# Kernel optimization log

Measured on AMD Instinct MI355X. Metric: run time of the kernel, lower is better.

Reference implementation:

```python
import jax, jax.numpy as jnp
import numpy as np

N = 65536   # num nodes
F = 512     # input feature dim
H = 256     # hid_dim
E = 1048576 # num edges (avg degree 16)
R = 512     # num_reps


def setup_inputs() -> dict:
    key = jax.random.key(0)
    ks = jax.random.split(key, 8)
    nodes = jax.random.normal(ks[0], (N, F), dtype=jnp.float32)
    c_nodes = jax.random.normal(ks[1], (N, F), dtype=jnp.float32)  # corrupted features
    senders = jax.random.randint(ks[2], (E,), 0, N, dtype=jnp.int32)
    receivers = jax.random.randint(ks[3], (E,), 0, N, dtype=jnp.int32)
    s = 1.0 / np.sqrt(F)
    W = jax.random.uniform(ks[4], (F, H), jnp.float32, -s, s)  # Dense kernel
    b = jnp.zeros((H,), jnp.float32)                            # Dense bias
    W_bilinear = jax.random.normal(ks[5], (H, H), jnp.float32) / np.sqrt(H)
    centers = jax.random.normal(ks[6], (R, H), jnp.float32)     # EucCluster param
    return dict(nodes=nodes, c_nodes=c_nodes, senders=senders, receivers=receivers,
                W=W, b=b, W_bilinear=W_bilinear, centers=centers)


def _gcn(x, senders, receivers, W, b):
    # jraph.GraphConvolution(Dense, add_self_edges=False, symmetric_normalization=True)
    x = x @ W + b  # [N,H]
    ones = jnp.ones((senders.shape[0],), x.dtype)
    deg_s = jax.ops.segment_sum(ones, senders, num_segments=N)
    x = x * jax.lax.rsqrt(jnp.maximum(deg_s, 1.0))[:, None]
    x = jax.ops.segment_sum(x[senders], receivers, num_segments=N)  # scatter-sum aggregation
    deg_r = jax.ops.segment_sum(ones, receivers, num_segments=N)
    x = x * jax.lax.rsqrt(jnp.maximum(deg_r, 1.0))[:, None]
    return jax.nn.selu(x)  # activation 'SeLU'


def reference(nodes, c_nodes, senders, receivers, W, b, W_bilinear, centers):
    # DGI with shared single-layer GCN (train=False path; single layer => no dropout)
    nodes1 = _gcn(nodes, senders, receivers, W, b)    # [N,H]
    nodes2 = _gcn(c_nodes, senders, receivers, W, b)  # [N,H]
    summary = jax.nn.sigmoid(jnp.mean(nodes1, axis=0))  # dgi_readout, [H]
    all_nodes = jnp.concatenate([nodes1, nodes2], axis=0)  # [2N,H]
    logits = (all_nodes @ W_bilinear) @ summary  # bilinear, [2N]
    # row L2-normalize embeddings
    emb = nodes1 / jnp.linalg.norm(nodes1, axis=1, keepdims=True)
    # Euclidean clustering: pairwise dists via GEMM trick
    d2 = (jnp.sum(emb * emb, axis=1)[:, None]
          + jnp.sum(centers * centers, axis=1)[None, :]
          - 2.0 * emb @ centers.T)  # [N,R]
    dists = jnp.sqrt(jnp.maximum(d2, 1e-12))
    cluster_dists = jnp.min(dists, axis=1)   # per-node dist to nearest center
    rep_ids = jnp.argmin(dists, axis=0)      # representative node per center
    cluster_loss = jnp.sum(cluster_dists)
    return emb, centers, rep_ids, cluster_loss, logits
```

## Files before the change

kernel.cpp:

```cpp
#include <hip/hip_runtime.h>
#include <math.h>

#define N_NODES 65536
#define F_DIM 512
#define H_DIM 256
#define E_EDGES 1048576
#define R_REPS 512

typedef _Float16 f16x8 __attribute__((ext_vector_type(8)));
typedef float f32x4_t __attribute__((ext_vector_type(4)));

__device__ __forceinline__ float selu_f(float x) {
    const float SC = 1.0507009873554804934f;
    const float AL = 1.6732632423543772848f;
    return x > 0.f ? SC * x : SC * AL * expm1f(x);
}

__device__ __forceinline__ void split8(const float* __restrict__ g, f16x8* hi, f16x8* lo) {
    float4 v0 = *(const float4*)g;
    float4 v1 = *(const float4*)(g + 4);
    f16x8 h, l;
    h[0] = (_Float16)v0.x; h[1] = (_Float16)v0.y; h[2] = (_Float16)v0.z; h[3] = (_Float16)v0.w;
    h[4] = (_Float16)v1.x; h[5] = (_Float16)v1.y; h[6] = (_Float16)v1.z; h[7] = (_Float16)v1.w;
    l[0] = (_Float16)(v0.x - (float)h[0]); l[1] = (_Float16)(v0.y - (float)h[1]);
    l[2] = (_Float16)(v0.z - (float)h[2]); l[3] = (_Float16)(v0.w - (float)h[3]);
    l[4] = (_Float16)(v1.x - (float)h[4]); l[5] = (_Float16)(v1.y - (float)h[5]);
    l[6] = (_Float16)(v1.z - (float)h[6]); l[7] = (_Float16)(v1.w - (float)h[7]);
    *hi = h; *lo = l;
}

__device__ __forceinline__ int wave_sort64(int v, int lane) {
    #pragma unroll
    for (int k = 2; k <= 64; k <<= 1) {
        #pragma unroll
        for (int j = k >> 1; j > 0; j >>= 1) {
            int p = __shfl_xor(v, j);
            bool takeMin = (((lane & j) == 0) == ((lane & k) == 0));
            int mn = min(v, p), mx = max(v, p);
            v = takeMin ? mn : mx;
        }
    }
    return v;
}

__global__ void k_init(int* cnt_s, int* cnt_r, float* colsum,
                       unsigned* node_min, unsigned long long* center_min,
                       double* loss_acc) {
    int i = blockIdx.x * 256 + threadIdx.x;
    if (i < N_NODES) { cnt_s[i] = 0; cnt_r[i] = 0; node_min[i] = 0x7F800000u; }
    if (i < H_DIM) colsum[i] = 0.f;
    if (i < R_REPS) center_min[i] = ~0ull;
    if (i == 0) *loss_acc = 0.0;
}

__global__ void k_degree(const int* __restrict__ senders, const int* __restrict__ receivers,
                         int* __restrict__ cnt_s, int* __restrict__ cnt_r) {
    int e = blockIdx.x * 256 + threadIdx.x;
    if (e < E_EDGES) {
        atomicAdd(&cnt_s[senders[e]], 1);
        atomicAdd(&cnt_r[receivers[e]], 1);
    }
}

__global__ void k_invsqrt(const int* __restrict__ cnt_s, const int* __restrict__ cnt_r,
                          float* __restrict__ inv_s, float* __restrict__ inv_r) {
    int i = blockIdx.x * 256 + threadIdx.x;
    if (i < N_NODES) {
        inv_s[i] = 1.0f / sqrtf(fmaxf((float)cnt_s[i], 1.f));
        inv_r[i] = 1.0f / sqrtf(fmaxf((float)cnt_r[i], 1.f));
    }
}

__global__ __launch_bounds__(1024) void k_scan(const int* __restrict__ cnt,
                                               int* __restrict__ row_ptr,
                                               int* __restrict__ cursor) {
    __shared__ int part[1024];
    int t = threadIdx.x;
    int base = t * 64;
    int s = 0;
    #pragma unroll 8
    for (int i = 0; i < 64; ++i) s += cnt[base + i];
    part[t] = s;
    __syncthreads();
    for (int off = 1; off < 1024; off <<= 1) {
        int other = (t >= off) ? part[t - off] : 0;
        __syncthreads();
        part[t] += other;
        __syncthreads();
    }
    int run = part[t] - s;
    for (int i = 0; i < 64; ++i) {
        row_ptr[base + i] = run;
        cursor[base + i] = run;
        run += cnt[base + i];
    }
    if (t == 1023) row_ptr[N_NODES] = run;
}

__global__ void k_fill(const int* __restrict__ senders, const int* __restrict__ receivers,
                       int* __restrict__ cursor, int* __restrict__ csr_send) {
    int e = blockIdx.x * 256 + threadIdx.x;
    if (e < E_EDGES) {
        int pos = atomicAdd(&cursor[receivers[e]], 1);
        csr_send[pos] = senders[e];
    }
}

__global__ void k_splitWT(const float* __restrict__ W, _Float16* __restrict__ hiT,
                          _Float16* __restrict__ loT) {
    int idx = blockIdx.x * 256 + threadIdx.x;
    int n = idx & (H_DIM - 1);
    int k = idx >> 8;
    float x = W[(size_t)k * H_DIM + n];
    _Float16 h = (_Float16)x;
    hiT[(size_t)n * F_DIM + k] = h;
    loT[(size_t)n * F_DIM + k] = (_Float16)(x - (float)h);
}

#define LDP 44

#define MFMA3(accv, AH, AL, BH, BL) \
    accv = __builtin_amdgcn_mfma_f32_16x16x32_f16(AH, BH, accv, 0, 0, 0); \
    accv = __builtin_amdgcn_mfma_f32_16x16x32_f16(AH, BL, accv, 0, 0, 0); \
    accv = __builtin_amdgcn_mfma_f32_16x16x32_f16(AL, BH, accv, 0, 0, 0);

#define MFMA_CORE \
    f16x8 ah[4], al[4]; \
    _Pragma("unroll") \
    for (int mi = 0; mi < 4; ++mi) { \
        ah[mi] = *(f16x8*)&Ah[wm * 64 + mi * 16 + lrow][kg * 8]; \
        al[mi] = *(f16x8*)&Al[wm * 64 + mi * 16 + lrow][kg * 8]; \
    } \
    _Pragma("unroll") \
    for (int ni = 0; ni < 4; ++ni) { \
        f16x8 bh = *(f16x8*)&Bh[wn * 64 + ni * 16 + lrow][kg * 8]; \
        f16x8 bl = *(f16x8*)&Bl[wn * 64 + ni * 16 + lrow][kg * 8]; \
        _Pragma("unroll") \
        for (int mi = 0; mi < 4; ++mi) { MFMA3(acc[mi][ni], ah[mi], al[mi], bh, bl) } \
    }

#define STAGE_A_F32(gA) { \
    f16x8 h0, l0, h1, l1; \
    split8((gA) + k0, &h0, &l0); \
    split8((gA) + k0 + 8, &h1, &l1); \
    *(f16x8*)&Ah[sr][skh] = h0; *(f16x8*)&Ah[sr][skh + 8] = h1; \
    *(f16x8*)&Al[sr][skh] = l0; *(f16x8*)&Al[sr][skh + 8] = l1; }

#define STAGE_B_F32(gB) { \
    f16x8 h0, l0, h1, l1; \
    split8((gB) + k0, &h0, &l0); \
    split8((gB) + k0 + 8, &h1, &l1); \
    *(f16x8*)&Bh[sr][skh] = h0; *(f16x8*)&Bh[sr][skh + 8] = h1; \
    *(f16x8*)&Bl[sr][skh] = l0; *(f16x8*)&Bl[sr][skh + 8] = l1; }

__global__ __launch_bounds__(256) void k_gemm_mfma(
    const float* __restrict__ A,
    const _Float16* __restrict__ BThi, const _Float16* __restrict__ BTlo,
    const float* __restrict__ bias, const float* __restrict__ inv_s,
    float* __restrict__ X, int K) {
    __shared__ _Float16 Ah[128][LDP], Al[128][LDP], Bh[128][LDP], Bl[128][LDP];
    const int t = threadIdx.x;
    const int lane = t & 63;
    const int wm = (t >> 6) >> 1, wn = (t >> 6) & 1;
    const int lrow = lane & 15, kg = lane >> 4;
    const int m0 = blockIdx.x * 128, n0 = blockIdx.y * 128;
    const int sr = t >> 1, skh = (t & 1) << 4;
    const float* gA = A + (size_t)(m0 + sr) * K + skh;
    const _Float16* gBh = BThi + (size_t)(n0 + sr) * K + skh;
    const _Float16* gBl = BTlo + (size_t)(n0 + sr) * K + skh;
    f32x4_t acc[4][4] = {};
    for (int k0 = 0; k0 < K; k0 += 32) {
        __syncthreads();
        STAGE_A_F32(gA)
        *(float4*)&Bh[sr][skh]     = *(const float4*)(gBh + k0);
        *(float4*)&Bh[sr][skh + 8] = *(const float4*)(gBh + k0 + 8);
        *(float4*)&Bl[sr][skh]     = *(const float4*)(gBl + k0);
        *(float4*)&Bl[sr][skh + 8] = *(const float4*)(gBl + k0 + 8);
        __syncthreads();
        MFMA_CORE
    }
    #pragma unroll
    for (int ni = 0; ni < 4; ++ni) {
        int col = n0 + wn * 64 + ni * 16 + lrow;
        float bc = bias[col];
        #pragma unroll
        for (int mi = 0; mi < 4; ++mi) {
            #pragma unroll
            for (int j = 0; j < 4; ++j) {
                int row = m0 + wm * 64 + mi * 16 + kg * 4 + j;
                X[(size_t)row * H_DIM + col] = (acc[mi][ni][j] + bc) * inv_s[row];
            }
        }
    }
}

__global__ __launch_bounds__(256) void k_cluster_mfma(
    const float* __restrict__ emb, const float* __restrict__ centers,
    const float* __restrict__ e2, const float* __restrict__ c2,
    unsigned* __restrict__ node_min, unsigned long long* __restrict__ center_min) {
    __shared__ _Float16 Ah[128][LDP], Al[128][LDP], Bh[128][LDP], Bl[128][LDP];
    __shared__ unsigned s_nmin[128];
    __shared__ unsigned long long s_cmin[128];
    const int t = threadIdx.x;
    const int lane = t & 63;
    const int wm = (t >> 6) >> 1, wn = (t >> 6) & 1;
    const int lrow = lane & 15, kg = lane >> 4;
    const int m0 = blockIdx.x * 128, n0 = blockIdx.y * 128;
    const int sr = t >> 1, skh = (t & 1) << 4;
    const int K = H_DIM;
    const float* gA = emb + (size_t)(m0 + sr) * K + skh;
    const float* gB = centers + (size_t)(n0 + sr) * K + skh;
    if (t < 128) { s_nmin[t] = 0x7F800000u; s_cmin[t] = ~0ull; }
    f32x4_t acc[4][4] = {};
    for (int k0 = 0; k0 < K; k0 += 32) {
        __syncthreads();
        STAGE_A_F32(gA)
        STAGE_B_F32(gB)
        __syncthreads();
        MFMA_CORE
    }
    float cv[4];
    #pragma unroll
    for (int ni = 0; ni < 4; ++ni) cv[ni] = c2[n0 + wn * 64 + ni * 16 + lrow];
    unsigned long long cb[4] = {~0ull, ~0ull, ~0ull, ~0ull};
    #pragma unroll
    for (int mi = 0; mi < 4; ++mi) {
        #pragma unroll
        for (int j = 0; j < 4; ++j) {
            int lr = wm * 64 + mi * 16 + kg * 4 + j;
            int row = m0 + lr;
            float ev = e2[row];
            float rmin = 3.402823466e+38f;
            #pragma unroll
            for (int ni = 0; ni < 4; ++ni) {
                float d2 = ev + cv[ni] - 2.f * acc[mi][ni][j];
                float d = sqrtf(fmaxf(d2, 1e-12f));
                rmin = fminf(rmin, d);
                unsigned long long pk = ((unsigned long long)__float_as_uint(d) << 32) | (unsigned)row;
                if (pk < cb[ni]) cb[ni] = pk;
            }
            atomicMin(&s_nmin[lr], __float_as_uint(rmin));
        }
    }
    #pragma unroll
    for (int ni = 0; ni < 4; ++ni)
        atomicMin(&s_cmin[wn * 64 + ni * 16 + lrow], cb[ni]);
    __syncthreads();
    if (t < 128) {
        atomicMin(&node_min[m0 + t], s_nmin[t]);
        atomicMin(&center_min[n0 + t], s_cmin[t]);
    }
}

__global__ __launch_bounds__(256) void k_agg1(
    const float* __restrict__ X, const int* __restrict__ csr_send,
    const int* __restrict__ row_ptr, const float* __restrict__ inv_r,
    float* __restrict__ out_emb) {
    int node = blockIdx.x * 4 + (threadIdx.x >> 6);
    int lane = threadIdx.x & 63;
    int beg = row_ptr[node], end = row_ptr[node + 1];
    float4 acc = {0.f, 0.f, 0.f, 0.f};
    for (int b = beg; b < end; b += 64) {
        int n = min(64, end - b);
        int myS = (lane < n) ? csr_send[b + lane] : 0x7FFFFFFF;
        myS = wave_sort64(myS, lane);
        for (int i = 0; i < n; ++i) {
            int s = __shfl(myS, i);
            float4 x = *(const float4*)&X[(size_t)s * H_DIM + (lane << 2)];
            acc.x += x.x; acc.y += x.y; acc.z += x.z; acc.w += x.w;
        }
    }
    float ir = inv_r[node];
    float4 o;
    o.x = selu_f(acc.x * ir);
    o.y = selu_f(acc.y * ir);
    o.z = selu_f(acc.z * ir);
    o.w = selu_f(acc.w * ir);
    *(float4*)&out_emb[(size_t)node * H_DIM + (lane << 2)] = o;
}

__global__ __launch_bounds__(256) void k_agg2(
    const float* __restrict__ X, const int* __restrict__ csr_send,
    const int* __restrict__ row_ptr, const float* __restrict__ inv_r,
    const float* __restrict__ v, float* __restrict__ out) {
    int node = blockIdx.x * 4 + (threadIdx.x >> 6);
    int lane = threadIdx.x & 63;
    int beg = row_ptr[node], end = row_ptr[node + 1];
    float4 acc = {0.f, 0.f, 0.f, 0.f};
    for (int b = beg; b < end; b += 64) {
        int n = min(64, end - b);
        int myS = (lane < n) ? csr_send[b + lane] : 0x7FFFFFFF;
        myS = wave_sort64(myS, lane);
        for (int i = 0; i < n; ++i) {
            int s = __shfl(myS, i);
            float4 x = *(const float4*)&X[(size_t)s * H_DIM + (lane << 2)];
            acc.x += x.x; acc.y += x.y; acc.z += x.z; acc.w += x.w;
        }
    }
    float ir = inv_r[node];
    float4 vv = *(const float4*)&v[lane << 2];
    float d = selu_f(acc.x * ir) * vv.x + selu_f(acc.y * ir) * vv.y
            + selu_f(acc.z * ir) * vv.z + selu_f(acc.w * ir) * vv.w;
    #pragma unroll
    for (int off = 32; off; off >>= 1) d += __shfl_down(d, off);
    if (lane == 0) out[node] = d;
}

__global__ __launch_bounds__(256) void k_colsum(const float* __restrict__ nodes1,
                                                float* __restrict__ colsum) {
    int t = threadIdx.x;
    size_t r0 = (size_t)blockIdx.x * 64;
    float s = 0.f;
    for (int r = 0; r < 64; ++r) s += nodes1[(r0 + r) * H_DIM + t];
    atomicAdd(&colsum[t], s);
}

__global__ void k_summary_v(const float* __restrict__ colsum, const float* __restrict__ Wb,
                            float* __restrict__ v) {
    __shared__ float s_sum[H_DIM];
    int t = threadIdx.x;
    float m = colsum[t] * (1.f / (float)N_NODES);
    s_sum[t] = 1.f / (1.f + expf(-m));
    __syncthreads();
    float acc = 0.f;
    for (int j = 0; j < H_DIM; ++j) acc += Wb[t * H_DIM + j] * s_sum[j];
    v[t] = acc;
}

__global__ __launch_bounds__(256) void k_normrow(
    float* __restrict__ emb, const float* __restrict__ v,
    float* __restrict__ logits, float* __restrict__ e2) {
    int row = blockIdx.x * 4 + (threadIdx.x >> 6);
    int lane = threadIdx.x & 63;
    float4 a = *(float4*)&emb[(size_t)row * H_DIM + (lane << 2)];
    float4 vv = *(const float4*)&v[lane << 2];
    float d = a.x * vv.x + a.y * vv.y + a.z * vv.z + a.w * vv.w;
    float ss = a.x * a.x + a.y * a.y + a.z * a.z + a.w * a.w;
    #pragma unroll
    for (int off = 32; off; off >>= 1) {
        d += __shfl_xor(d, off);
        ss += __shfl_xor(ss, off);
    }
    if (lane == 0) logits[row] = d;
    float inv = 1.f / sqrtf(ss);
    a.x *= inv; a.y *= inv; a.z *= inv; a.w *= inv;
    *(float4*)&emb[(size_t)row * H_DIM + (lane << 2)] = a;
    float s2 = a.x * a.x + a.y * a.y + a.z * a.z + a.w * a.w;
    #pragma unroll
    for (int off = 32; off; off >>= 1) s2 += __shfl_xor(s2, off);
    if (lane == 0) e2[row] = s2;
}

__global__ __launch_bounds__(256) void k_c2(const float* __restrict__ centers,
                                            float* __restrict__ c2) {
    int row = blockIdx.x * 4 + (threadIdx.x >> 6);
    int lane = threadIdx.x & 63;
    float4 a = *(const float4*)&centers[(size_t)row * H_DIM + (lane << 2)];
    float ss = a.x * a.x + a.y * a.y + a.z * a.z + a.w * a.w;
    #pragma unroll
    for (int off = 32; off; off >>= 1) ss += __shfl_xor(ss, off);
    if (lane == 0) c2[row] = ss;
}

__global__ __launch_bounds__(256) void k_loss(const unsigned* __restrict__ node_min,
                                              double* __restrict__ acc) {
    int i = blockIdx.x * 256 + threadIdx.x;
    float s = __uint_as_float(node_min[i]);
    #pragma unroll
    for (int off = 32; off; off >>= 1) s += __shfl_down(s, off);
    __shared__ float ws[4];
    int lane = threadIdx.x & 63, w = threadIdx.x >> 6;
    if (lane == 0) ws[w] = s;
    __syncthreads();
    if (threadIdx.x == 0) {
        float tot = ws[0] + ws[1] + ws[2] + ws[3];
        atomicAdd(acc, (double)tot);
    }
}

__global__ void k_finalize(const unsigned long long* __restrict__ center_min,
                           const double* __restrict__ loss_acc,
                           float* __restrict__ rep_out, float* __restrict__ loss_out) {
    int t = blockIdx.x * 256 + threadIdx.x;
    if (t < R_REPS) rep_out[t] = (float)(unsigned)(center_min[t] & 0xFFFFFFFFull);
    if (t == 0) *loss_out = (float)(*loss_acc);
}

extern "C" void kernel_launch(void* const* d_in, const int* in_sizes, int n_in,
                              void* d_out, int out_size, void* d_ws, size_t ws_size,
                              hipStream_t stream) {
    const float* nodes   = (const float*)d_in[0];
    const float* c_nodes = (const float*)d_in[1];
    const int* senders   = (const int*)d_in[2];
    const int* receivers = (const int*)d_in[3];
    const float* W       = (const float*)d_in[4];
    const float* bias    = (const float*)d_in[5];
    const float* Wb      = (const float*)d_in[6];
    const float* centers = (const float*)d_in[7];

    float* out = (float*)d_out;
    float* out_emb    = out;
    float* out_cent   = out + (size_t)N_NODES * H_DIM;
    float* out_rep    = out_cent + (size_t)R_REPS * H_DIM;
    float* out_loss   = out_rep + R_REPS;
    float* out_logits = out_loss + 1;

    char* wp = (char*)d_ws;
    unsigned long long* center_min = (unsigned long long*)wp; wp += (size_t)R_REPS * 8;
    double* loss_acc = (double*)wp;             wp += 8;
    float* X = (float*)wp;                      wp += (size_t)N_NODES * H_DIM * 4;
    int* csr_send = (int*)wp;                   wp += (size_t)E_EDGES * 4;
    int* row_ptr = (int*)wp;                    wp += (size_t)(N_NODES + 2) * 4;
    int* cursor = (int*)wp;                     wp += (size_t)N_NODES * 4;
    int* cnt_s = (int*)wp;                      wp += (size_t)N_NODES * 4;
    int* cnt_r = (int*)wp;                      wp += (size_t)N_NODES * 4;
    float* inv_s = (float*)wp;                  wp += (size_t)N_NODES * 4;
    float* inv_r = (float*)wp;                  wp += (size_t)N_NODES * 4;
    float* colsum = (float*)wp;                 wp += (size_t)H_DIM * 4;
    float* v = (float*)wp;                      wp += (size_t)H_DIM * 4;
    float* e2 = (float*)wp;                     wp += (size_t)N_NODES * 4;
    float* c2 = (float*)wp;                     wp += (size_t)R_REPS * 4;
    unsigned* node_min = (unsigned*)wp;         wp += (size_t)N_NODES * 4;
    _Float16* WhiT = (_Float16*)wp;             wp += (size_t)H_DIM * F_DIM * 2;
    _Float16* WloT = (_Float16*)wp;             wp += (size_t)H_DIM * F_DIM * 2;

    k_init<<<N_NODES / 256, 256, 0, stream>>>(cnt_s, cnt_r, colsum, node_min, center_min, loss_acc);
    k_degree<<<E_EDGES / 256, 256, 0, stream>>>(senders, receivers, cnt_s, cnt_r);
    k_invsqrt<<<N_NODES / 256, 256, 0, stream>>>(cnt_s, cnt_r, inv_s, inv_r);
    k_scan<<<1, 1024, 0, stream>>>(cnt_r, row_ptr, cursor);
    k_fill<<<E_EDGES / 256, 256, 0, stream>>>(senders, receivers, cursor, csr_send);
    k_splitWT<<<(F_DIM * H_DIM) / 256, 256, 0, stream>>>(W, WhiT, WloT);

    dim3 gg(N_NODES / 128, H_DIM / 128);
    k_gemm_mfma<<<gg, 256, 0, stream>>>(nodes, WhiT, WloT, bias, inv_s, X, F_DIM);
    k_agg1<<<N_NODES / 4, 256, 0, stream>>>(X, csr_send, row_ptr, inv_r, out_emb);

    k_colsum<<<N_NODES / 64, 256, 0, stream>>>(out_emb, colsum);
    k_summary_v<<<1, 256, 0, stream>>>(colsum, Wb, v);
    k_normrow<<<N_NODES / 4, 256, 0, stream>>>(out_emb, v, out_logits, e2);
    k_c2<<<R_REPS / 4, 256, 0, stream>>>(centers, c2);

    dim3 gc(N_NODES / 128, R_REPS / 128);
    k_cluster_mfma<<<gc, 256, 0, stream>>>(out_emb, centers, e2, c2, node_min, center_min);
    k_loss<<<N_NODES / 256, 256, 0, stream>>>(node_min, loss_acc);
    k_finalize<<<2, 256, 0, stream>>>(center_min, loss_acc, out_rep, out_loss);
    hipMemcpyAsync(out_cent, centers, (size_t)R_REPS * H_DIM * 4, hipMemcpyDeviceToDevice, stream);

    k_gemm_mfma<<<gg, 256, 0, stream>>>(c_nodes, WhiT, WloT, bias, inv_s, X, F_DIM);
    k_agg2<<<N_NODES / 4, 256, 0, stream>>>(X, csr_send, row_ptr, inv_r, v, out_logits + N_NODES);
}
```

Measured before the change: 894.4 us.

## Prefetch next A tile into registers during MFMA in GEMM and cluster kernels

Both MFMA GEMM kernels now load the next K-slice of the fp32 A operand into registers before running the MFMA core on the current slice, then split and write it to shared memory after a barrier. This register-level software prefetch is meant to hide global-load latency behind matrix work. The B operand is still loaded after compute. The shared-memory row pitch is also reduced from 44 to 36 halves, which changes the bank-conflict pattern and LDS footprint, and the extra live registers may lower occupancy.

```diff
diff --git a/kernel.cpp b/kernel.cpp
--- a/kernel.cpp
+++ b/kernel.cpp
@@ -16,9 +16,7 @@
     return x > 0.f ? SC * x : SC * AL * expm1f(x);
 }
 
-__device__ __forceinline__ void split8(const float* __restrict__ g, f16x8* hi, f16x8* lo) {
-    float4 v0 = *(const float4*)g;
-    float4 v1 = *(const float4*)(g + 4);
+__device__ __forceinline__ void split8v(float4 v0, float4 v1, f16x8* hi, f16x8* lo) {
     f16x8 h, l;
     h[0] = (_Float16)v0.x; h[1] = (_Float16)v0.y; h[2] = (_Float16)v0.z; h[3] = (_Float16)v0.w;
     h[4] = (_Float16)v1.x; h[5] = (_Float16)v1.y; h[6] = (_Float16)v1.z; h[7] = (_Float16)v1.w;
@@ -117,7 +115,7 @@
     loT[(size_t)n * F_DIM + k] = (_Float16)(x - (float)h);
 }
 
-#define LDP 44
+#define LDP 36
 
 #define MFMA3(accv, AH, AL, BH, BL) \
     accv = __builtin_amdgcn_mfma_f32_16x16x32_f16(AH, BH, accv, 0, 0, 0); \
@@ -139,19 +137,12 @@
         for (int mi = 0; mi < 4; ++mi) { MFMA3(acc[mi][ni], ah[mi], al[mi], bh, bl) } \
     }
 
-#define STAGE_A_F32(gA) { \
+#define WRITE_A_REGS { \
     f16x8 h0, l0, h1, l1; \
-    split8((gA) + k0, &h0, &l0); \
-    split8((gA) + k0 + 8, &h1, &l1); \
+    split8v(pa0, pa1, &h0, &l0); \
+    split8v(pa2, pa3, &h1, &l1); \
     *(f16x8*)&Ah[sr][skh] = h0; *(f16x8*)&Ah[sr][skh + 8] = h1; \
     *(f16x8*)&Al[sr][skh] = l0; *(f16x8*)&Al[sr][skh + 8] = l1; }
-
-#define STAGE_B_F32(gB) { \
-    f16x8 h0, l0, h1, l1; \
-    split8((gB) + k0, &h0, &l0); \
-    split8((gB) + k0 + 8, &h1, &l1); \
-    *(f16x8*)&Bh[sr][skh] = h0; *(f16x8*)&Bh[sr][skh + 8] = h1; \
-    *(f16x8*)&Bl[sr][skh] = l0; *(f16x8*)&Bl[sr][skh + 8] = l1; }
 
 __global__ __launch_bounds__(256) void k_gemm_mfma(
     const float* __restrict__ A,
@@ -169,15 +160,32 @@
     const _Float16* gBh = BThi + (size_t)(n0 + sr) * K + skh;
     const _Float16* gBl = BTlo + (size_t)(n0 + sr) * K + skh;
     f32x4_t acc[4][4] = {};
+    float4 pa0, pa1, pa2, pa3;
+    pa0 = *(const float4*)(gA + 0);  pa1 = *(const float4*)(gA + 4);
+    pa2 = *(const float4*)(gA + 8);  pa3 = *(const float4*)(gA + 12);
+    WRITE_A_REGS
+    *(float4*)&Bh[sr][skh]     = *(const float4*)(gBh + 0);
+    *(float4*)&Bh[sr][skh + 8] = *(const float4*)(gBh + 8);
+    *(float4*)&Bl[sr][skh]     = *(const float4*)(gBl + 0);
+    *(float4*)&Bl[sr][skh + 8] = *(const float4*)(gBl + 8);
     for (int k0 = 0; k0 < K; k0 += 32) {
         __syncthreads();
-        STAGE_A_F32(gA)
-        *(float4*)&Bh[sr][skh]     = *(const float4*)(gBh + k0);
-        *(float4*)&Bh[sr][skh + 8] = *(const float4*)(gBh + k0 + 8);
-        *(float4*)&Bl[sr][skh]     = *(const float4*)(gBl + k0);
-        *(float4*)&Bl[sr][skh + 8] = *(const float4*)(gBl + k0 + 8);
-        __syncthreads();
+        const bool more = (k0 + 32) < K;
+        if (more) {
+            pa0 = *(const float4*)(gA + k0 + 32);
+            pa1 = *(const float4*)(gA + k0 + 36);
+            pa2 = *(const float4*)(gA + k0 + 40);
+            pa3 = *(const float4*)(gA + k0 + 44);
+        }
         MFMA_CORE
+        __syncthreads();
+        if (more) {
+            WRITE_A_REGS
+            *(float4*)&Bh[sr][skh]     = *(const float4*)(gBh + k0 + 32);
+            *(float4*)&Bh[sr][skh + 8] = *(const float4*)(gBh + k0 + 40);
+            *(float4*)&Bl[sr][skh]     = *(const float4*)(gBl + k0 + 32);
+            *(float4*)&Bl[sr][skh + 8] = *(const float4*)(gBl + k0 + 40);
+        }
     }
     #pragma unroll
     for (int ni = 0; ni < 4; ++ni) {
@@ -212,12 +220,40 @@
     const float* gB = centers + (size_t)(n0 + sr) * K + skh;
     if (t < 128) { s_nmin[t] = 0x7F800000u; s_cmin[t] = ~0ull; }
     f32x4_t acc[4][4] = {};
+    float4 pa0, pa1, pa2, pa3;
+    pa0 = *(const float4*)(gA + 0);  pa1 = *(const float4*)(gA + 4);
+    pa2 = *(const float4*)(gA + 8);  pa3 = *(const float4*)(gA + 12);
+    WRITE_A_REGS
+    {
+        f16x8 h0, l0, h1, l1;
+        float4 b0 = *(const float4*)(gB + 0), b1 = *(const float4*)(gB + 4);
+        float4 b2 = *(const float4*)(gB + 8), b3 = *(const float4*)(gB + 12);
+        split8v(b0, b1, &h0, &l0);
+        split8v(b2, b3, &h1, &l1);
+        *(f16x8*)&Bh[sr][skh] = h0; *(f16x8*)&Bh[sr][skh + 8] = h1;
+        *(f16x8*)&Bl[sr][skh] = l0; *(f16x8*)&Bl[sr][skh + 8] = l1;
+    }
     for (int k0 = 0; k0 < K; k0 += 32) {
         __syncthreads();
-        STAGE_A_F32(gA)
-        STAGE_B_F32(gB)
-        __syncthreads();
+        const bool more = (k0 + 32) < K;
+        if (more) {
+            pa0 = *(const float4*)(gA + k0 + 32);
+            pa1 = *(const float4*)(gA + k0 + 36);
+            pa2 = *(const float4*)(gA + k0 + 40);
+            pa3 = *(const float4*)(gA + k0 + 44);
+        }
         MFMA_CORE
+        __syncthreads();
+        if (more) {
+            WRITE_A_REGS
+            f16x8 h0, l0, h1, l1;
+            float4 b0 = *(const float4*)(gB + k0 + 32), b1 = *(const float4*)(gB + k0 + 36);
+            float4 b2 = *(const float4*)(gB + k0 + 40), b3 = *(const float4*)(gB + k0 + 44);
+            split8v(b0, b1, &h0, &l0);
+            split8v(b2, b3, &h1, &l1);
+            *(f16x8*)&Bh[sr][skh] = h0; *(f16x8*)&Bh[sr][skh + 8] = h1;
+            *(f16x8*)&Bl[sr][skh] = l0; *(f16x8*)&Bl[sr][skh + 8] = l1;
+        }
     }
     float cv[4];
     #pragma unroll
```

Result: no change. 891.4 us (-0.3%).
